# Performance work log

Measured on AMD Instinct MI355X. Metric: run time of the kernel, lower is better.

The kernel has to match this reference:

```python
import jax, jax.numpy as jnp
import numpy as np

N = 100000   # nodes
E = 300000   # directed edges (avg degree 3, molecular graphs)
G = 4000     # molecules in the batch
IN = 9
HID = 128
HEADS = 4
NEG_SLOPE = 0.2


def setup_inputs() -> dict:
    key = jax.random.key(0)
    ks = jax.random.split(key, 12)
    x = jax.random.normal(ks[0], (N, IN), dtype=jnp.float32)
    edge_index = jax.random.randint(ks[1], (2, E), 0, N, dtype=jnp.int32)
    batch = jnp.sort(jax.random.randint(ks[2], (N,), 0, G, dtype=jnp.int32))
    s = 0.1  # keep activations in a sane range
    W1 = jax.random.normal(ks[3], (IN, HEADS * HID), dtype=jnp.float32) * s
    a_src1 = jax.random.normal(ks[4], (HEADS, HID), dtype=jnp.float32) * s
    a_dst1 = jax.random.normal(ks[5], (HEADS, HID), dtype=jnp.float32) * s
    b1 = jax.random.normal(ks[6], (HEADS * HID,), dtype=jnp.float32) * s
    W2 = jax.random.normal(ks[7], (HEADS * HID, HID), dtype=jnp.float32) * s
    a_src2 = jax.random.normal(ks[8], (1, HID), dtype=jnp.float32) * s
    a_dst2 = jax.random.normal(ks[9], (1, HID), dtype=jnp.float32) * s
    b2 = jax.random.normal(ks[10], (HID,), dtype=jnp.float32) * s
    return {"x": x, "edge_index": edge_index, "batch": batch,
            "W1": W1, "a_src1": a_src1, "a_dst1": a_dst1, "b1": b1,
            "W2": W2, "a_src2": a_src2, "a_dst2": a_dst2, "b2": b2}


def _gat_conv(x, edge_index, W, a_src, a_dst, b, heads, out_ch, concat):
    """PyG GATConv: linear proj, per-edge leaky-relu attention logits,
    segment softmax over destination nodes, scatter-add aggregation.
    add_self_loops=True (PyG default)."""
    n = x.shape[0]
    loops = jnp.arange(n, dtype=edge_index.dtype)
    src = jnp.concatenate([edge_index[0], loops])
    dst = jnp.concatenate([edge_index[1], loops])

    h = (x @ W).reshape(n, heads, out_ch)                  # [N, H, C]
    alpha_s = jnp.einsum('nhc,hc->nh', h, a_src)           # [N, H]
    alpha_d = jnp.einsum('nhc,hc->nh', h, a_dst)           # [N, H]

    logits = jax.nn.leaky_relu(alpha_s[src] + alpha_d[dst], NEG_SLOPE)  # [Etot, H]
    # numerically stable segment softmax over incoming edges of each dst
    m = jax.ops.segment_max(logits, dst, num_segments=n)   # [N, H] (finite: self-loops)
    e = jnp.exp(logits - m[dst])
    z = jax.ops.segment_sum(e, dst, num_segments=n)
    alpha = e / (z[dst] + 1e-16)                           # [Etot, H]

    msg = h[src] * alpha[:, :, None]                       # [Etot, H, C]
    out = jax.ops.segment_sum(msg, dst, num_segments=n)    # [N, H, C]
    if concat:
        out = out.reshape(n, heads * out_ch)
    else:
        out = out.mean(axis=1)
    return out + b


def reference(x, edge_index, batch, W1, a_src1, a_dst1, b1, W2, a_src2, a_dst2, b2):
    h = jax.nn.elu(_gat_conv(x, edge_index, W1, a_src1, a_dst1, b1, HEADS, HID, True))
    h = jax.nn.elu(_gat_conv(h, edge_index, W2, a_src2, a_dst2, b2, 1, HID, True))
    # global mean pool per graph
    sums = jax.ops.segment_sum(h, batch, num_segments=G)   # [G, HID]
    cnt = jax.ops.segment_sum(jnp.ones((h.shape[0],), h.dtype), batch, num_segments=G)
    return sums / jnp.maximum(cnt, 1.0)[:, None]
```

## Files before the change

kernel.cpp:

```cpp
#include <hip/hip_runtime.h>

#define N_NODES 100000
#define N_EDGES 300000
#define N_GRAPHS 4000
#define CAP 32

typedef float f32x4 __attribute__((ext_vector_type(4)));
typedef float f32x16 __attribute__((ext_vector_type(16)));
typedef __bf16 bf16x8 __attribute__((ext_vector_type(8)));
typedef __bf16 bf16x4 __attribute__((ext_vector_type(4)));
typedef __bf16 bf16x2 __attribute__((ext_vector_type(2)));
typedef _Float16 f16x8 __attribute__((ext_vector_type(8)));

static const size_t OFF_XA    = 0;
static const size_t OFF_AD4   = OFF_XA + (size_t)N_NODES * 16;
static const size_t OFF_P2B   = OFF_AD4 + (size_t)N_NODES * 4;
static const size_t OFF_ASAD2 = OFF_P2B + (size_t)N_NODES * 64;
static const size_t OFF_WSB   = OFF_ASAD2 + (size_t)N_NODES * 2;
static const size_t OFF_W1B   = OFF_WSB + 32768;
static const size_t OFF_GST   = OFF_W1B + 4096;
static const size_t OFF_INT   = OFF_GST + 4096;

#define PRE_NODE_END 391
#define PRE_PACKB_END 455
#define PRE_W1B_END 487
#define PRE_GST_END 503
#define PRE_BKT_END 1675

__device__ __forceinline__ float lrelu(float x) { return x < 0.f ? 0.2f * x : x; }
__device__ __forceinline__ float elu(float x)   { return x > 0.f ? x : __expf(x) - 1.f; }

__global__ __launch_bounds__(256) void k_pre(
    const float* __restrict__ x, const float* __restrict__ W1,
    const float* __restrict__ a_src1, const float* __restrict__ a_dst1,
    const float* __restrict__ W2, const int* __restrict__ batch,
    const int* __restrict__ ei,
    float* __restrict__ xa, float* __restrict__ ad4,
    __bf16* __restrict__ wsB, _Float16* __restrict__ w1b,
    int* __restrict__ deg, int* __restrict__ bucket, int* __restrict__ gstart) {
    int b = blockIdx.x, tid = threadIdx.x;
    if (b < PRE_NODE_END) {
        __shared__ float wf[72];
        if (tid < 72) {
            int isd = tid / 36, r = tid % 36, k = r / 4, h = r % 4;
            const float* a = isd ? a_dst1 : a_src1;
            float s = 0.f;
            for (int c = 0; c < 128; c++) s += W1[k * 512 + h * 128 + c] * a[h * 128 + c];
            wf[tid] = s;
        }
        __syncthreads();
        int n = b * 256 + tid;
        if (n >= N_NODES) return;
        float xv[9];
#pragma unroll
        for (int k = 0; k < 9; k++) xv[k] = x[n * 9 + k];
        float as[4], ad[4];
#pragma unroll
        for (int h = 0; h < 4; h++) {
            float s = 0.f, d = 0.f;
#pragma unroll
            for (int k = 0; k < 9; k++) {
                s += xv[k] * wf[k * 4 + h];
                d += xv[k] * wf[36 + k * 4 + h];
            }
            as[h] = s; ad[h] = d;
        }
        f32x4* xp = (f32x4*)(xa + (size_t)n * 16);
        xp[0] = (f32x4){xv[0], xv[1], xv[2], xv[3]};
        xp[1] = (f32x4){xv[4], xv[5], xv[6], xv[7]};
        xp[2] = (f32x4){xv[8], as[0], as[1], as[2]};
        xp[3] = (f32x4){as[3], 0.f, 0.f, 0.f};
        *(f32x4*)(ad4 + (size_t)n * 4) = (f32x4){ad[0], ad[1], ad[2], ad[3]};
    } else if (b < PRE_PACKB_END) {
        int t = (b - PRE_NODE_END) * 256 + tid;
#pragma unroll
        for (int m = 0; m < 4; m++) {
            int idx = t * 4 + m;
            int k = idx >> 7, nn = idx & 127;
            wsB[(size_t)nn * 512 + k] = (__bf16)W2[(size_t)k * 128 + nn];
        }
    } else if (b < PRE_W1B_END) {
        int t = (b - PRE_PACKB_END) * 256 + tid;
        int j = t >> 4, k = t & 15;
        w1b[t] = (k < 9) ? (_Float16)W1[(size_t)k * 512 + j] : (_Float16)0.f;
    } else if (b < PRE_GST_END) {
        int g = (b - PRE_W1B_END) * 256 + tid;
        if (g > N_GRAPHS) return;
        int lo = 0, hi = N_NODES;
        while (lo < hi) { int mid = (lo + hi) >> 1; if (batch[mid] < g) lo = mid + 1; else hi = mid; }
        gstart[g] = lo;
    } else {
        int e = (b - PRE_GST_END) * 256 + tid;
        if (e >= N_EDGES) return;
        int s = ei[e], d = ei[N_EDGES + e];
        int slot = atomicAdd(&deg[d], 1);
        if (slot < CAP) bucket[d * CAP + slot] = s;
    }
}

__global__ __launch_bounds__(512, 6) void k_gemm(
    const float* __restrict__ xa, const float* __restrict__ ad4,
    const int* __restrict__ deg, const int* __restrict__ bucket,
    const _Float16* __restrict__ w1b, const float* __restrict__ b1,
    const __bf16* __restrict__ wsB,
    const float* __restrict__ a_src2, const float* __restrict__ a_dst2,
    __bf16* __restrict__ p2b, float* __restrict__ asad2) {
    __shared__ __bf16 As[64 * 128];
    __shared__ _Float16 AgF[4 * 64 * 24];
    float* red2 = (float*)AgF;
    const int tid = threadIdx.x;
    const int lane = tid & 63;
    const int w = tid >> 6;
    const int i = lane & 15;
    const int q = lane >> 4;
    const int m0 = blockIdx.x * 64;

    {
        const int r = tid >> 3, sub = tid & 7;
        const int hp = sub & 1;
        const int slot = sub >> 1;
        const int n = m0 + r;
        float acc[2][9] = {};
        float z[2] = {};
        const bool valid = (n < N_NODES);
        if (valid) {
            const float2 adv = *(const float2*)(ad4 + (size_t)n * 4 + hp * 2);
            int dg = deg[n];
            if (dg > CAP) dg = CAP;
#define GATHER1(SRC) do {                                                    \
            const f32x4* xp_ = (const f32x4*)(xa + (size_t)(SRC) * 16);      \
            f32x4 v0 = xp_[0], v1 = xp_[1], v2 = xp_[2], v3 = xp_[3];        \
            float as0 = hp ? v2.w : v2.y;                                    \
            float as1 = hp ? v3.x : v2.z;                                    \
            float e0 = __expf(lrelu(as0 + adv.x));                           \
            float e1 = __expf(lrelu(as1 + adv.y));                           \
            z[0] += e0; z[1] += e1;                                          \
            float xs[9] = {v0.x, v0.y, v0.z, v0.w, v1.x, v1.y, v1.z, v1.w, v2.x}; \
            _Pragma("unroll")                                                \
            for (int k = 0; k < 9; k++) {                                    \
                acc[0][k] += e0 * xs[k]; acc[1][k] += e1 * xs[k];            \
            }                                                                \
        } while (0)
            if (slot == 3) GATHER1(n);
            int j = slot;
            int srcn = (j < dg) ? bucket[n * CAP + j] : -1;
            while (srcn >= 0) {
                int src = srcn;
                j += 4;
                srcn = (j < dg) ? bucket[n * CAP + j] : -1;
                GATHER1(src);
            }
#undef GATHER1
        }
#pragma unroll
        for (int off = 2; off <= 4; off <<= 1) {
#pragma unroll
            for (int h = 0; h < 2; h++) {
                z[h] += __shfl_xor(z[h], off);
#pragma unroll
                for (int k = 0; k < 9; k++) acc[h][k] += __shfl_xor(acc[h][k], off);
            }
        }
        if (sub < 2) {
#pragma unroll
            for (int hh = 0; hh < 2; hh++) {
                float inv = valid ? 1.f / z[hh] : 0.f;
                f16x8 p0, p1;
#pragma unroll
                for (int k = 0; k < 8; k++) { p0[k] = (_Float16)(acc[hh][k] * inv); p1[k] = (_Float16)0.f; }
                p1[0] = (_Float16)(acc[hh][8] * inv);
                _Float16* dst = AgF + (size_t)((sub * 2 + hh) * 64 + r) * 24;
                *(f16x8*)dst = p0;
                *(f16x8*)(dst + 8) = p1;
            }
        }
    }
    __syncthreads();

    f32x4 acc[4];
#pragma unroll
    for (int r = 0; r < 4; r++) acc[r] = (f32x4){0.f, 0.f, 0.f, 0.f};

    const __bf16* bcol = wsB + (size_t)(w * 16 + i) * 512 + q * 8;
    const int nt = w & 1, jt = w >> 1;
    const int l31 = lane & 31, qh = lane >> 5;
    const int ilw = lane & 15, hw = (lane >> 4) & 1;

#pragma unroll
    for (int pass = 0; pass < 4; pass++) {
        bf16x8 breg[4];
#pragma unroll
        for (int kc = 0; kc < 4; kc++)
            breg[kc] = *(const bf16x8*)(bcol + pass * 128 + kc * 32);

        {
            f16x8 av = *(const f16x8*)(w1b + ((size_t)(pass * 128 + jt * 32 + l31) * 16 + qh * 8));
            f16x8 bv = *(const f16x8*)&AgF[(size_t)(pass * 64 + nt * 32 + l31) * 24 + qh * 8];
            f32x16 cfr = (f32x16){0.f, 0.f, 0.f, 0.f, 0.f, 0.f, 0.f, 0.f,
                                  0.f, 0.f, 0.f, 0.f, 0.f, 0.f, 0.f, 0.f};
            cfr = __builtin_amdgcn_mfma_f32_32x32x16_f16(av, bv, cfr, 0, 0, 0);
#pragma unroll
            for (int r2 = 0; r2 < 4; r2++) {
                f32x4 b1v = *(const f32x4*)(b1 + pass * 128 + jt * 32 + r2 * 8 + qh * 4);
                bf16x4 pk;
#pragma unroll
                for (int m = 0; m < 4; m++) pk[m] = (__bf16)elu(cfr[r2 * 4 + m] + b1v[m]);
                *(bf16x4*)&As[(size_t)(((nt * 2 + hw) * 4 + jt) * 512 +
                                       (r2 * 16 + ilw) * 8 + qh * 4)] = pk;
            }
        }
        __syncthreads();

#pragma unroll
        for (int kc = 0; kc < 4; kc++) {
#pragma unroll
            for (int rt = 0; rt < 4; rt++) {
                bf16x8 af = *(const bf16x8*)&As[(rt * 4 + kc) * 512 + lane * 8];
                acc[rt] = __builtin_amdgcn_mfma_f32_16x16x32_bf16(af, breg[kc], acc[rt], 0, 0, 0);
            }
        }
        __syncthreads();
    }

    float as2 = a_src2[w * 16 + i];
    float ad2 = a_dst2[w * 16 + i];
#pragma unroll
    for (int rt = 0; rt < 4; rt++) {
#pragma unroll
        for (int qq = 0; qq < 4; qq++) {
            int r2 = rt * 16 + q * 4 + qq;
            float v = acc[rt][qq];
            if (m0 + r2 < N_NODES)
                p2b[(size_t)(m0 + r2) * 128 + w * 16 + i] = (__bf16)v;
            float s = v * as2, d = v * ad2;
#pragma unroll
            for (int off = 1; off < 16; off <<= 1) {
                s += __shfl_xor(s, off);
                d += __shfl_xor(d, off);
            }
            if (i == 0) {
                red2[r2 * 16 + w * 2] = s;
                red2[r2 * 16 + w * 2 + 1] = d;
            }
        }
    }
    __syncthreads();
    if (tid < 128) {
        int r2 = tid >> 1, cc = tid & 1;
        float sum = 0.f;
#pragma unroll
        for (int ww = 0; ww < 8; ww++) sum += red2[r2 * 16 + ww * 2 + cc];
        if (m0 + r2 < N_NODES) asad2[(size_t)(m0 + r2) * 2 + cc] = sum;
    }
}

__global__ __launch_bounds__(256) void k_agg2pool(
    const __bf16* __restrict__ p2b, const float* __restrict__ asad2,
    const int* __restrict__ deg, const int* __restrict__ bucket,
    const float* __restrict__ b2, const int* __restrict__ gstart,
    float* __restrict__ out) {
    __shared__ float red[4 * 128];
    int g = blockIdx.x;
    int tid = threadIdx.x;
    int wv = __builtin_amdgcn_readfirstlane(tid >> 6);
    int lane = tid & 63;
    int s0n = gstart[g], e0n = gstart[g + 1];
    float b2a = b2[2 * lane], b2b = b2[2 * lane + 1];
    float g0 = 0.f, g1 = 0.f;
    for (int n = s0n + wv; n < e0n; n += 4) {
        float ad = asad2[n * 2 + 1];
        float e = __expf(lrelu(asad2[n * 2] + ad));
        float z = e;
        bf16x2 v = ((const bf16x2*)(p2b + (size_t)n * 128))[lane];
        float a0 = e * (float)v.x;
        float a1 = e * (float)v.y;
        int dg = deg[n];
        if (dg > CAP) dg = CAP;
        for (int j = 0; j < dg; j += 4) {
            int s0 = bucket[n * CAP + j];
            int s1 = bucket[n * CAP + min(j + 1, dg - 1)];
            int s2 = bucket[n * CAP + min(j + 2, dg - 1)];
            int s3 = bucket[n * CAP + min(j + 3, dg - 1)];
            float l0 = asad2[s0 * 2], l1 = asad2[s1 * 2];
            float l2 = asad2[s2 * 2], l3 = asad2[s3 * 2];
            bf16x2 w0 = ((const bf16x2*)(p2b + (size_t)s0 * 128))[lane];
            bf16x2 w1 = ((const bf16x2*)(p2b + (size_t)s1 * 128))[lane];
            bf16x2 w2 = ((const bf16x2*)(p2b + (size_t)s2 * 128))[lane];
            bf16x2 w3 = ((const bf16x2*)(p2b + (size_t)s3 * 128))[lane];
            float e0 = __expf(lrelu(l0 + ad));
            float e1 = (j + 1 < dg) ? __expf(lrelu(l1 + ad)) : 0.f;
            float e2 = (j + 2 < dg) ? __expf(lrelu(l2 + ad)) : 0.f;
            float e3 = (j + 3 < dg) ? __expf(lrelu(l3 + ad)) : 0.f;
            z += e0 + e1 + e2 + e3;
            a0 += e0 * (float)w0.x + e1 * (float)w1.x + e2 * (float)w2.x + e3 * (float)w3.x;
            a1 += e0 * (float)w0.y + e1 * (float)w1.y + e2 * (float)w2.y + e3 * (float)w3.y;
        }
        float inv = 1.f / z;
        g0 += elu(a0 * inv + b2a);
        g1 += elu(a1 * inv + b2b);
    }
    red[wv * 128 + 2 * lane] = g0;
    red[wv * 128 + 2 * lane + 1] = g1;
    __syncthreads();
    if (tid < 128) {
        float sum = red[tid] + red[128 + tid] + red[256 + tid] + red[384 + tid];
        int cnt = e0n - s0n;
        out[(size_t)g * 128 + tid] = sum / (float)(cnt > 0 ? cnt : 1);
    }
}

extern "C" void kernel_launch(void* const* d_in, const int* in_sizes, int n_in,
                              void* d_out, int out_size, void* d_ws, size_t ws_size,
                              hipStream_t stream) {
    const float* x       = (const float*)d_in[0];
    const int*   ei      = (const int*)d_in[1];
    const int*   batch   = (const int*)d_in[2];
    const float* W1      = (const float*)d_in[3];
    const float* a_src1  = (const float*)d_in[4];
    const float* a_dst1  = (const float*)d_in[5];
    const float* b1      = (const float*)d_in[6];
    const float* W2      = (const float*)d_in[7];
    const float* a_src2  = (const float*)d_in[8];
    const float* a_dst2  = (const float*)d_in[9];
    const float* b2      = (const float*)d_in[10];
    float* out = (float*)d_out;

    float* wsf   = (float*)d_ws;
    float* xa    = wsf + OFF_XA;
    float* ad4   = wsf + OFF_AD4;
    __bf16* p2b  = (__bf16*)(wsf + OFF_P2B);
    float* asad2 = wsf + OFF_ASAD2;
    __bf16* wsB  = (__bf16*)(wsf + OFF_WSB);
    _Float16* w1b = (_Float16*)(wsf + OFF_W1B);
    int* gstart  = (int*)(wsf + OFF_GST);
    int* wsi    = (int*)(wsf + OFF_INT);
    int* deg    = wsi;
    int* bucket = wsi + N_NODES;

    hipMemsetAsync(deg, 0, N_NODES * sizeof(int), stream);
    k_pre<<<PRE_BKT_END, 256, 0, stream>>>(x, W1, a_src1, a_dst1, W2, batch, ei,
                                           xa, ad4, wsB, w1b, deg, bucket, gstart);
    k_gemm<<<(N_NODES + 63) / 64, 512, 0, stream>>>(xa, ad4, deg, bucket, w1b, b1,
                                                    wsB, a_src2, a_dst2, p2b, asad2);
    k_agg2pool<<<N_GRAPHS, 256, 0, stream>>>(p2b, asad2, deg, bucket, b2, gstart, out);
}
```

Before: 194.0 us.

## Chain layer-1 MFMA output directly into layer-2 MFMA in registers, fold bias into GEMM

Restructures the fused GEMM so that each wave computes a 32x32 tile of the layer-1 projection (ELU applied in registers) and feeds it straight into a 32x32x16 bf16 MFMA as the B operand, removing the shared-memory staging buffer and its barriers. W1 columns are permuted so the accumulator layout matches the next MFMA's operand layout, and bias b1 is folded into the first GEMM via a constant-one input column. W2 is stored transposed for the new access pattern, and the attention-logit reduction uses a new padded shared array. Occupancy hint drops to 4 blocks per CU, which may allow more registers but fewer resident waves.

```diff
diff --git a/kernel.cpp b/kernel.cpp
--- a/kernel.cpp
+++ b/kernel.cpp
@@ -16,8 +16,8 @@
 static const size_t OFF_AD4   = OFF_XA + (size_t)N_NODES * 16;
 static const size_t OFF_P2B   = OFF_AD4 + (size_t)N_NODES * 4;
 static const size_t OFF_ASAD2 = OFF_P2B + (size_t)N_NODES * 64;
-static const size_t OFF_WSB   = OFF_ASAD2 + (size_t)N_NODES * 2;
-static const size_t OFF_W1B   = OFF_WSB + 32768;
+static const size_t OFF_W2T   = OFF_ASAD2 + (size_t)N_NODES * 2;
+static const size_t OFF_W1B   = OFF_W2T + 32768;
 static const size_t OFF_GST   = OFF_W1B + 4096;
 static const size_t OFF_INT   = OFF_GST + 4096;
 
@@ -30,13 +30,19 @@
 __device__ __forceinline__ float lrelu(float x) { return x < 0.f ? 0.2f * x : x; }
 __device__ __forceinline__ float elu(float x)   { return x > 0.f ? x : __expf(x) - 1.f; }
 
+__device__ __forceinline__ int pi_j(int j) {
+    int l = j & 15;
+    int d = (l >= 4 && l < 8) ? 4 : (l >= 8 && l < 12) ? -4 : 0;
+    return j + d;
+}
+
 __global__ __launch_bounds__(256) void k_pre(
     const float* __restrict__ x, const float* __restrict__ W1,
     const float* __restrict__ a_src1, const float* __restrict__ a_dst1,
-    const float* __restrict__ W2, const int* __restrict__ batch,
-    const int* __restrict__ ei,
+    const float* __restrict__ W2, const float* __restrict__ b1,
+    const int* __restrict__ batch, const int* __restrict__ ei,
     float* __restrict__ xa, float* __restrict__ ad4,
-    __bf16* __restrict__ wsB, _Float16* __restrict__ w1b,
+    __bf16* __restrict__ w2t, _Float16* __restrict__ w1b,
     int* __restrict__ deg, int* __restrict__ bucket, int* __restrict__ gstart) {
     int b = blockIdx.x, tid = threadIdx.x;
     if (b < PRE_NODE_END) {
@@ -76,13 +82,15 @@
 #pragma unroll
         for (int m = 0; m < 4; m++) {
             int idx = t * 4 + m;
-            int k = idx >> 7, nn = idx & 127;
-            wsB[(size_t)nn * 512 + k] = (__bf16)W2[(size_t)k * 128 + nn];
+            int c = idx >> 9, j = idx & 511;
+            w2t[idx] = (__bf16)W2[(size_t)j * 128 + c];
         }
     } else if (b < PRE_W1B_END) {
         int t = (b - PRE_PACKB_END) * 256 + tid;
         int j = t >> 4, k = t & 15;
-        w1b[t] = (k < 9) ? (_Float16)W1[(size_t)k * 512 + j] : (_Float16)0.f;
+        int jp = pi_j(j);
+        float v = (k < 9) ? W1[(size_t)k * 512 + jp] : (k == 9) ? b1[jp] : 0.f;
+        w1b[t] = (_Float16)v;
     } else if (b < PRE_GST_END) {
         int g = (b - PRE_W1B_END) * 256 + tid;
         if (g > N_GRAPHS) return;
@@ -98,21 +106,21 @@
     }
 }
 
-__global__ __launch_bounds__(512, 6) void k_gemm(
+__global__ __launch_bounds__(512, 4) void k_gemm(
     const float* __restrict__ xa, const float* __restrict__ ad4,
     const int* __restrict__ deg, const int* __restrict__ bucket,
-    const _Float16* __restrict__ w1b, const float* __restrict__ b1,
-    const __bf16* __restrict__ wsB,
+    const _Float16* __restrict__ w1b, const __bf16* __restrict__ w2t,
     const float* __restrict__ a_src2, const float* __restrict__ a_dst2,
     __bf16* __restrict__ p2b, float* __restrict__ asad2) {
-    __shared__ __bf16 As[64 * 128];
     __shared__ _Float16 AgF[4 * 64 * 24];
-    float* red2 = (float*)AgF;
+    __shared__ float red[64 * 34];
     const int tid = threadIdx.x;
     const int lane = tid & 63;
     const int w = tid >> 6;
-    const int i = lane & 15;
-    const int q = lane >> 4;
+    const int l31 = lane & 31;
+    const int qh = lane >> 5;
+    const int ct = w >> 1;
+    const int nt = w & 1;
     const int m0 = blockIdx.x * 64;
 
     {
@@ -120,7 +128,7 @@
         const int hp = sub & 1;
         const int slot = sub >> 1;
         const int n = m0 + r;
-        float acc[2][9] = {};
+        float acc0[2][9] = {};
         float z[2] = {};
         const bool valid = (n < N_NODES);
         if (valid) {
@@ -138,7 +146,7 @@
             float xs[9] = {v0.x, v0.y, v0.z, v0.w, v1.x, v1.y, v1.z, v1.w, v2.x}; \
             _Pragma("unroll")                                                \
             for (int k = 0; k < 9; k++) {                                    \
-                acc[0][k] += e0 * xs[k]; acc[1][k] += e1 * xs[k];            \
+                acc0[0][k] += e0 * xs[k]; acc0[1][k] += e1 * xs[k];          \
             }                                                                \
         } while (0)
             if (slot == 3) GATHER1(n);
@@ -158,7 +166,7 @@
             for (int h = 0; h < 2; h++) {
                 z[h] += __shfl_xor(z[h], off);
 #pragma unroll
-                for (int k = 0; k < 9; k++) acc[h][k] += __shfl_xor(acc[h][k], off);
+                for (int k = 0; k < 9; k++) acc0[h][k] += __shfl_xor(acc0[h][k], off);
             }
         }
         if (sub < 2) {
@@ -167,8 +175,9 @@
                 float inv = valid ? 1.f / z[hh] : 0.f;
                 f16x8 p0, p1;
 #pragma unroll
-                for (int k = 0; k < 8; k++) { p0[k] = (_Float16)(acc[hh][k] * inv); p1[k] = (_Float16)0.f; }
-                p1[0] = (_Float16)(acc[hh][8] * inv);
+                for (int k = 0; k < 8; k++) { p0[k] = (_Float16)(acc0[hh][k] * inv); p1[k] = (_Float16)0.f; }
+                p1[0] = (_Float16)(acc0[hh][8] * inv);
+                p1[1] = (_Float16)1.f;
                 _Float16* dst = AgF + (size_t)((sub * 2 + hh) * 64 + r) * 24;
                 *(f16x8*)dst = p0;
                 *(f16x8*)(dst + 8) = p1;
@@ -177,80 +186,61 @@
     }
     __syncthreads();
 
-    f32x4 acc[4];
-#pragma unroll
-    for (int r = 0; r < 4; r++) acc[r] = (f32x4){0.f, 0.f, 0.f, 0.f};
-
-    const __bf16* bcol = wsB + (size_t)(w * 16 + i) * 512 + q * 8;
-    const int nt = w & 1, jt = w >> 1;
-    const int l31 = lane & 31, qh = lane >> 5;
-    const int ilw = lane & 15, hw = (lane >> 4) & 1;
-
-#pragma unroll
-    for (int pass = 0; pass < 4; pass++) {
-        bf16x8 breg[4];
-#pragma unroll
-        for (int kc = 0; kc < 4; kc++)
-            breg[kc] = *(const bf16x8*)(bcol + pass * 128 + kc * 32);
-
-        {
-            f16x8 av = *(const f16x8*)(w1b + ((size_t)(pass * 128 + jt * 32 + l31) * 16 + qh * 8));
-            f16x8 bv = *(const f16x8*)&AgF[(size_t)(pass * 64 + nt * 32 + l31) * 24 + qh * 8];
+    f32x16 acc = (f32x16){0.f, 0.f, 0.f, 0.f, 0.f, 0.f, 0.f, 0.f,
+                          0.f, 0.f, 0.f, 0.f, 0.f, 0.f, 0.f, 0.f};
+    const _Float16* avbase = w1b + (size_t)l31 * 16 + qh * 8;
+    const __bf16* w2base = w2t + (size_t)(ct * 32 + l31) * 512 + qh * 8;
+
+    for (int head = 0; head < 4; head++) {
+        f16x8 agB = *(const f16x8*)&AgF[(size_t)(head * 64 + nt * 32 + l31) * 24 + qh * 8];
+#pragma unroll
+        for (int jbl = 0; jbl < 4; jbl++) {
+            const int jb = head * 4 + jbl;
+            f16x8 av = *(const f16x8*)(avbase + (size_t)jb * 512);
             f32x16 cfr = (f32x16){0.f, 0.f, 0.f, 0.f, 0.f, 0.f, 0.f, 0.f,
                                   0.f, 0.f, 0.f, 0.f, 0.f, 0.f, 0.f, 0.f};
-            cfr = __builtin_amdgcn_mfma_f32_32x32x16_f16(av, bv, cfr, 0, 0, 0);
-#pragma unroll
-            for (int r2 = 0; r2 < 4; r2++) {
-                f32x4 b1v = *(const f32x4*)(b1 + pass * 128 + jt * 32 + r2 * 8 + qh * 4);
-                bf16x4 pk;
-#pragma unroll
-                for (int m = 0; m < 4; m++) pk[m] = (__bf16)elu(cfr[r2 * 4 + m] + b1v[m]);
-                *(bf16x4*)&As[(size_t)(((nt * 2 + hw) * 4 + jt) * 512 +
-                                       (r2 * 16 + ilw) * 8 + qh * 4)] = pk;
-            }
-        }
-        __syncthreads();
-
-#pragma unroll
-        for (int kc = 0; kc < 4; kc++) {
-#pragma unroll
-            for (int rt = 0; rt < 4; rt++) {
-                bf16x8 af = *(const bf16x8*)&As[(rt * 4 + kc) * 512 + lane * 8];
-                acc[rt] = __builtin_amdgcn_mfma_f32_16x16x32_bf16(af, breg[kc], acc[rt], 0, 0, 0);
-            }
-        }
-        __syncthreads();
-    }
-
-    float as2 = a_src2[w * 16 + i];
-    float ad2 = a_dst2[w * 16 + i];
-#pragma unroll
-    for (int rt = 0; rt < 4; rt++) {
-#pragma unroll
-        for (int qq = 0; qq < 4; qq++) {
-            int r2 = rt * 16 + q * 4 + qq;
-            float v = acc[rt][qq];
-            if (m0 + r2 < N_NODES)
-                p2b[(size_t)(m0 + r2) * 128 + w * 16 + i] = (__bf16)v;
-            float s = v * as2, d = v * ad2;
-#pragma unroll
-            for (int off = 1; off < 16; off <<= 1) {
-                s += __shfl_xor(s, off);
-                d += __shfl_xor(d, off);
-            }
-            if (i == 0) {
-                red2[r2 * 16 + w * 2] = s;
-                red2[r2 * 16 + w * 2 + 1] = d;
-            }
-        }
-    }
+            cfr = __builtin_amdgcn_mfma_f32_32x32x16_f16(av, agB, cfr, 0, 0, 0);
+            float ve[16];
+#pragma unroll
+            for (int r = 0; r < 16; r++) ve[r] = elu(cfr[r]);
+#pragma unroll
+            for (int sp = 0; sp < 2; sp++) {
+                bf16x8 bfr;
+#pragma unroll
+                for (int e = 0; e < 8; e++) bfr[e] = (__bf16)ve[8 * sp + e];
+                bf16x8 afr = *(const bf16x8*)(w2base + (size_t)(jb * 32 + sp * 16));
+                acc = __builtin_amdgcn_mfma_f32_32x32x16_bf16(afr, bfr, acc, 0, 0, 0);
+            }
+        }
+    }
+
+    const int node = nt * 32 + l31;
+    const bool nvalid = (m0 + node < N_NODES);
+    float s = 0.f, d = 0.f;
+#pragma unroll
+    for (int Q = 0; Q < 4; Q++) {
+        f32x4 as2q = *(const f32x4*)(a_src2 + ct * 32 + Q * 8 + qh * 4);
+        f32x4 ad2q = *(const f32x4*)(a_dst2 + ct * 32 + Q * 8 + qh * 4);
+        bf16x4 pk;
+#pragma unroll
+        for (int m = 0; m < 4; m++) {
+            float v = acc[Q * 4 + m];
+            pk[m] = (__bf16)v;
+            s += v * as2q[m];
+            d += v * ad2q[m];
+        }
+        if (nvalid)
+            *(bf16x4*)(p2b + (size_t)(m0 + node) * 128 + ct * 32 + Q * 8 + qh * 4) = pk;
+    }
+    red[node * 34 + ct * 2 + qh] = s;
+    red[node * 34 + 17 + ct * 2 + qh] = d;
     __syncthreads();
     if (tid < 128) {
-        int r2 = tid >> 1, cc = tid & 1;
+        int n2 = tid >> 1, cc = tid & 1;
         float sum = 0.f;
 #pragma unroll
-        for (int ww = 0; ww < 8; ww++) sum += red2[r2 * 16 + ww * 2 + cc];
-        if (m0 + r2 < N_NODES) asad2[(size_t)(m0 + r2) * 2 + cc] = sum;
+        for (int sl = 0; sl < 8; sl++) sum += red[n2 * 34 + cc * 17 + sl];
+        if (m0 + n2 < N_NODES) asad2[(size_t)(m0 + n2) * 2 + cc] = sum;
     }
 }
 
@@ -330,7 +320,7 @@
     float* ad4   = wsf + OFF_AD4;
     __bf16* p2b  = (__bf16*)(wsf + OFF_P2B);
     float* asad2 = wsf + OFF_ASAD2;
-    __bf16* wsB  = (__bf16*)(wsf + OFF_WSB);
+    __bf16* w2t  = (__bf16*)(wsf + OFF_W2T);
     _Float16* w1b = (_Float16*)(wsf + OFF_W1B);
     int* gstart  = (int*)(wsf + OFF_GST);
     int* wsi    = (int*)(wsf + OFF_INT);
@@ -338,9 +328,9 @@
     int* bucket = wsi + N_NODES;
 
     hipMemsetAsync(deg, 0, N_NODES * sizeof(int), stream);
-    k_pre<<<PRE_BKT_END, 256, 0, stream>>>(x, W1, a_src1, a_dst1, W2, batch, ei,
-                                           xa, ad4, wsB, w1b, deg, bucket, gstart);
-    k_gemm<<<(N_NODES + 63) / 64, 512, 0, stream>>>(xa, ad4, deg, bucket, w1b, b1,
-                                                    wsB, a_src2, a_dst2, p2b, asad2);
+    k_pre<<<PRE_BKT_END, 256, 0, stream>>>(x, W1, a_src1, a_dst1, W2, b1, batch, ei,
+                                           xa, ad4, w2t, w1b, deg, bucket, gstart);
+    k_gemm<<<(N_NODES + 63) / 64, 512, 0, stream>>>(xa, ad4, deg, bucket, w1b, w2t,
+                                                    a_src2, a_dst2, p2b, asad2);
     k_agg2pool<<<N_GRAPHS, 256, 0, stream>>>(p2b, asad2, deg, bucket, b2, gstart, out);
 }
```

Result: slower. 210.1 us (+8.3%).
